# Performance work log

Hardware: AMD Instinct MI355X
Metric: run time of the kernel (lower is better)

Reference implementation:

```python
import jax, jax.numpy as jnp
import numpy as np

B, S, D = 4, 512, 256
H_SP, W_SP = 64, 64
NUM_HEADS = 8
HEAD_DIM = D // NUM_HEADS


def setup_inputs() -> dict:
    key = jax.random.key(0)
    ks = jax.random.split(key, 10)
    scale = 1.0 / np.sqrt(D)
    return {
        "query": jax.random.normal(ks[0], (B, S, D), dtype=jnp.float32),
        "key_value": jax.random.normal(ks[1], (B, D, H_SP, W_SP), dtype=jnp.float32),
        "Wq": jax.random.normal(ks[2], (D, D), dtype=jnp.float32) * scale,
        "bq": jnp.zeros((D,), dtype=jnp.float32),
        "Wk": jax.random.normal(ks[3], (D, D), dtype=jnp.float32) * scale,
        "bk": jnp.zeros((D,), dtype=jnp.float32),
        "Wv": jax.random.normal(ks[4], (D, D), dtype=jnp.float32) * scale,
        "bv": jnp.zeros((D,), dtype=jnp.float32),
        "Wo": jax.random.normal(ks[5], (D, D), dtype=jnp.float32) * scale,
        "bo": jnp.zeros((D,), dtype=jnp.float32),
    }


def reference(query, key_value, Wq, bq, Wk, bk, Wv, bv, Wo, bo):
    # query: (B, S, D); key_value: (B, D, H, W)
    b, d, h, w = key_value.shape
    s = query.shape[1]
    hw = h * w
    kv = key_value.reshape(b, d, hw).transpose(0, 2, 1)  # (B, HW, D)

    # Linear projections (torch Linear: x @ W.T + b)
    Q = query @ Wq.T + bq                                # (B, S, D)
    K = kv @ Wk.T + bk                                   # (B, HW, D)
    V = kv @ Wv.T + bv                                   # (B, HW, D)

    # Split heads: (B, nH, len, hd)
    Qh = Q.reshape(b, s, NUM_HEADS, HEAD_DIM).transpose(0, 2, 1, 3)
    Kh = K.reshape(b, hw, NUM_HEADS, HEAD_DIM).transpose(0, 2, 1, 3)
    Vh = V.reshape(b, hw, NUM_HEADS, HEAD_DIM).transpose(0, 2, 1, 3)

    scale = HEAD_DIM ** -0.5
    # NOTE: _add_spatial_attention is dead code (returns attn unchanged);
    # norm1/norm2 are never applied in forward; dropout is identity in eval.
    attn = jnp.einsum('bhsd,bhkd->bhsk', Qh, Kh) * scale  # (B, nH, S, HW)
    attn = jax.nn.softmax(attn, axis=-1)
    out = jnp.einsum('bhsk,bhkd->bhsd', attn, Vh)         # (B, nH, S, hd)
    out = out.transpose(0, 2, 1, 3).reshape(b, s, d)      # (B, S, D)
    return out @ Wo.T + bo
```

## Files before the change

kernel.cpp:

```cpp
#include <hip/hip_runtime.h>

constexpr int B_  = 4;
constexpr int S_  = 512;
constexpr int D_  = 256;
constexpr int HW_ = 4096;
constexpr int NH_ = 8;
constexpr int HD_ = 32;
constexpr int NSPLIT = 4;
constexpr int ROWS_  = B_ * NH_ * S_;
constexpr int KVB    = 64;
constexpr int TILES  = HW_ / NSPLIT / KVB;

typedef float  f32x4   __attribute__((ext_vector_type(4)));
typedef float  f32x16  __attribute__((ext_vector_type(16)));
typedef short  s16x4   __attribute__((ext_vector_type(4)));
typedef short  s16x8   __attribute__((ext_vector_type(8)));
typedef __bf16 bf16x8  __attribute__((ext_vector_type(8)));
typedef unsigned int u32x2 __attribute__((ext_vector_type(2)));
typedef unsigned int u32x4 __attribute__((ext_vector_type(4)));

__device__ __forceinline__ f32x4 mfma_bf16(s16x8 a, s16x8 b, f32x4 c) {
  return __builtin_amdgcn_mfma_f32_16x16x32_bf16(
      __builtin_bit_cast(bf16x8, a), __builtin_bit_cast(bf16x8, b), c, 0, 0, 0);
}
__device__ __forceinline__ f32x16 mfma32(s16x8 a, s16x8 b, f32x16 c) {
  return __builtin_amdgcn_mfma_f32_32x32x16_bf16(
      __builtin_bit_cast(bf16x8, a), __builtin_bit_cast(bf16x8, b), c, 0, 0, 0);
}

__device__ __forceinline__ void split4(float4 v, s16x4& h, s16x4& l) {
  float x[4] = {v.x, v.y, v.z, v.w};
  #pragma unroll
  for (int j = 0; j < 4; ++j) {
    unsigned xb = __float_as_uint(x[j]);
    h[j] = (short)(xb >> 16);
    float lo = x[j] - __uint_as_float(xb & 0xFFFF0000u);
    l[j] = (short)((__float_as_uint(lo) + 0x8000u) >> 16);
  }
}

__device__ __forceinline__ unsigned pk_hi(float x, float y) {
  return (__float_as_uint(x) >> 16) | (__float_as_uint(y) & 0xFFFF0000u);
}
__device__ __forceinline__ unsigned pk_lo(float x, float y) {
  float rx = x - __uint_as_float(__float_as_uint(x) & 0xFFFF0000u);
  float ry = y - __uint_as_float(__float_as_uint(y) & 0xFFFF0000u);
  return (__float_as_uint(rx) >> 16) | (__float_as_uint(ry) & 0xFFFF0000u);
}

__global__ __launch_bounds__(256)
void transpose_split(const float* __restrict__ KV,
                     short* __restrict__ Th, short* __restrict__ Tl)
{
  __shared__ float tile[64][65];
  const int bid = blockIdx.x;
  const int hwb = bid & 63;
  const int db  = (bid >> 6) & 3;
  const int b   = bid >> 8;
  const int hw0 = hwb * 64, d0 = db * 64;
  const int tid = threadIdx.x;
  #pragma unroll
  for (int i = 0; i < 4; ++i) {
    const int idx = tid + (i << 8);
    const int d = idx >> 4, h4 = idx & 15;
    *(float4*)&tile[d][h4 * 4] =
        *(const float4*)&KV[((size_t)(b * D_ + d0 + d)) * HW_ + hw0 + h4 * 4];
  }
  __syncthreads();
  #pragma unroll
  for (int i = 0; i < 4; ++i) {
    const int idx = tid + (i << 8);
    const int hw = idx >> 4, d4 = idx & 15;
    const float4 v = make_float4(tile[d4*4+0][hw], tile[d4*4+1][hw],
                                 tile[d4*4+2][hw], tile[d4*4+3][hw]);
    s16x4 hh, ll; split4(v, hh, ll);
    const size_t o = ((size_t)(b * HW_ + hw0 + hw)) * D_ + d0 + d4 * 4;
    *(s16x4*)&Th[o] = hh; *(s16x4*)&Tl[o] = ll;
  }
}

template<bool ASPLIT, bool DUAL, bool OSPLIT>
__global__ __launch_bounds__(256)
void gemm_mfma(const float* __restrict__ Af,
               const short* __restrict__ Ah_, const short* __restrict__ Al_,
               const float* __restrict__ W0, const float* __restrict__ b0,
               float* __restrict__ C0f, short* __restrict__ C0h, short* __restrict__ C0l,
               const float* __restrict__ W1, const float* __restrict__ b1,
               short* __restrict__ C1h, short* __restrict__ C1l,
               int M, float alpha)
{
  union Sm {
    struct {
      short Ah[64][40], Al[64][40];
      short W0h[64][40], W0l[64][40];
      short W1h[64][40], W1l[64][40];
    } s;
    float ep[64][76];
  };
  __shared__ __align__(16) Sm sm;

  const int tid = threadIdx.x;
  const int wv = tid >> 6, lane = tid & 63, lq = lane & 15, lg = lane >> 4;
  const int wm = wv >> 1, wn = wv & 1;
  const int nx = M >> 6;
  int bid = blockIdx.x;
  bid = (bid & 7) * ((nx << 2) >> 3) + (bid >> 3);
  const int xm = bid % nx, yn = bid / nx;
  const int m0 = xm << 6, n0 = yn << 6;

  f32x4 acc0[2][2] = {};
  f32x4 acc1[2][2] = {};

  s16x8 aH, aL;
  float4 aF[2], w0R[2], w1R[2];

  auto gload = [&](int kt) {
    const int k0 = kt << 5;
    if constexpr (ASPLIT) {
      const int m = tid >> 2, c8 = tid & 3;
      const size_t off = (size_t)(m0 + m) * D_ + k0 + c8 * 8;
      aH = *(const s16x8*)&Ah_[off];
      aL = *(const s16x8*)&Al_[off];
    } else {
      #pragma unroll
      for (int i = 0; i < 2; ++i) {
        const int idx = tid + (i << 8);
        const int m = idx >> 3, c4 = idx & 7;
        aF[i] = *(const float4*)&Af[(size_t)(m0 + m) * D_ + k0 + c4 * 4];
      }
    }
    #pragma unroll
    for (int i = 0; i < 2; ++i) {
      const int idx = tid + (i << 8);
      const int n = idx >> 3, c4 = idx & 7;
      w0R[i] = *(const float4*)&W0[(size_t)(n0 + n) * D_ + k0 + c4 * 4];
      if constexpr (DUAL)
        w1R[i] = *(const float4*)&W1[(size_t)(n0 + n) * D_ + k0 + c4 * 4];
    }
  };

  auto stage = [&]() {
    if constexpr (ASPLIT) {
      const int m = tid >> 2, c8 = tid & 3;
      *(s16x8*)&sm.s.Ah[m][c8 * 8] = aH;
      *(s16x8*)&sm.s.Al[m][c8 * 8] = aL;
    } else {
      #pragma unroll
      for (int i = 0; i < 2; ++i) {
        const int idx = tid + (i << 8);
        const int m = idx >> 3, c4 = idx & 7;
        s16x4 hh, ll; split4(aF[i], hh, ll);
        *(s16x4*)&sm.s.Ah[m][c4 * 4] = hh;
        *(s16x4*)&sm.s.Al[m][c4 * 4] = ll;
      }
    }
    #pragma unroll
    for (int i = 0; i < 2; ++i) {
      const int idx = tid + (i << 8);
      const int n = idx >> 3, c4 = idx & 7;
      float4 w = w0R[i];
      w.x *= alpha; w.y *= alpha; w.z *= alpha; w.w *= alpha;
      s16x4 hh, ll; split4(w, hh, ll);
      *(s16x4*)&sm.s.W0h[n][c4 * 4] = hh;
      *(s16x4*)&sm.s.W0l[n][c4 * 4] = ll;
      if constexpr (DUAL) {
        split4(w1R[i], hh, ll);
        *(s16x4*)&sm.s.W1h[n][c4 * 4] = hh;
        *(s16x4*)&sm.s.W1l[n][c4 * 4] = ll;
      }
    }
  };

  gload(0);
  #pragma unroll
  for (int kt = 0; kt < 8; ++kt) {
    __syncthreads();
    stage();
    __syncthreads();
    if (kt < 7) gload(kt + 1);
    s16x8 ah[2], al[2];
    #pragma unroll
    for (int mi = 0; mi < 2; ++mi) {
      ah[mi] = *(const s16x8*)&sm.s.Ah[wm * 32 + mi * 16 + lq][lg * 8];
      al[mi] = *(const s16x8*)&sm.s.Al[wm * 32 + mi * 16 + lq][lg * 8];
    }
    #pragma unroll
    for (int ni = 0; ni < 2; ++ni) {
      const int nr = wn * 32 + ni * 16 + lq;
      const s16x8 bh = *(const s16x8*)&sm.s.W0h[nr][lg * 8];
      const s16x8 bl = *(const s16x8*)&sm.s.W0l[nr][lg * 8];
      #pragma unroll
      for (int mi = 0; mi < 2; ++mi) {
        acc0[mi][ni] = mfma_bf16(ah[mi], bh, acc0[mi][ni]);
        acc0[mi][ni] = mfma_bf16(al[mi], bh, acc0[mi][ni]);
        acc0[mi][ni] = mfma_bf16(ah[mi], bl, acc0[mi][ni]);
      }
      if constexpr (DUAL) {
        const s16x8 ch = *(const s16x8*)&sm.s.W1h[nr][lg * 8];
        const s16x8 cl = *(const s16x8*)&sm.s.W1l[nr][lg * 8];
        #pragma unroll
        for (int mi = 0; mi < 2; ++mi) {
          acc1[mi][ni] = mfma_bf16(ah[mi], ch, acc1[mi][ni]);
          acc1[mi][ni] = mfma_bf16(al[mi], ch, acc1[mi][ni]);
          acc1[mi][ni] = mfma_bf16(ah[mi], cl, acc1[mi][ni]);
        }
      }
    }
  }

  __syncthreads();
  #pragma unroll
  for (int mi = 0; mi < 2; ++mi)
    #pragma unroll
    for (int ni = 0; ni < 2; ++ni)
      #pragma unroll
      for (int r = 0; r < 4; ++r)
        sm.ep[wm*32 + mi*16 + lg*4 + r][wn*32 + ni*16 + lq] = acc0[mi][ni][r];
  __syncthreads();
  #pragma unroll
  for (int i = 0; i < 4; ++i) {
    const int idx = tid + (i << 8);
    const int m = idx >> 4, c4 = idx & 15;
    const float4 v = *(const float4*)&sm.ep[m][c4 * 4];
    const float4 bb = *(const float4*)&b0[n0 + c4 * 4];
    const float4 o = make_float4(v.x + alpha * bb.x, v.y + alpha * bb.y,
                                 v.z + alpha * bb.z, v.w + alpha * bb.w);
    const size_t off = (size_t)(m0 + m) * D_ + n0 + c4 * 4;
    if constexpr (OSPLIT) {
      s16x4 hh, ll; split4(o, hh, ll);
      *(s16x4*)&C0h[off] = hh;
      *(s16x4*)&C0l[off] = ll;
    } else {
      *(float4*)&C0f[off] = o;
    }
  }

  if constexpr (DUAL) {
    __syncthreads();
    #pragma unroll
    for (int mi = 0; mi < 2; ++mi)
      #pragma unroll
      for (int ni = 0; ni < 2; ++ni)
        *(f32x4*)&sm.ep[wn*32 + ni*16 + lq][wm*32 + mi*16 + lg*4] = acc1[mi][ni];
    __syncthreads();
    const int b = m0 >> 12, hw0 = m0 & (HW_ - 1);
    #pragma unroll
    for (int i = 0; i < 4; ++i) {
      const int idx = tid + (i << 8);
      const int n = idx >> 4, m4 = idx & 15;
      const float4 v = *(const float4*)&sm.ep[n][m4 * 4];
      const float bb = b1[n0 + n];
      const float4 o = make_float4(v.x + bb, v.y + bb, v.z + bb, v.w + bb);
      s16x4 hh, ll; split4(o, hh, ll);
      const size_t off = ((size_t)(b * D_ + n0 + n)) * HW_ + hw0 + m4 * 4;
      *(s16x4*)&C1h[off] = hh;
      *(s16x4*)&C1l[off] = ll;
    }
  }
}

__global__ __launch_bounds__(256)
void attn_mfma32(const short* __restrict__ Qh_, const short* __restrict__ Ql_,
                 const short* __restrict__ Kh_, const short* __restrict__ Kl_,
                 const short* __restrict__ Vth, const short* __restrict__ Vtl,
                 float* __restrict__ Opart, float* __restrict__ Ml)
{
  union Sm {
    short V[2][2][32][72];
    float ep[4][32][33];
  };
  __shared__ __align__(16) Sm sm;

  const int tid  = threadIdx.x;
  const int wv   = tid >> 6, lane = tid & 63;
  const int lq   = lane & 31, hi = lane >> 5;

  int w = blockIdx.x;
  w = (w & 7) * 64 + (w >> 3);
  const int qt = w & 3;
  const int h  = (w >> 2) & 7;
  const int b  = (w >> 5) & 3;
  const int sp = w >> 7;
  const int q0 = qt * 128 + wv * 32;

  s16x8 qh[2], ql[2];
  {
    const size_t qb = ((size_t)(b * S_ + q0 + lq)) * D_ + h * HD_ + hi * 8;
    qh[0] = *(const s16x8*)&Qh_[qb];      qh[1] = *(const s16x8*)&Qh_[qb + 16];
    ql[0] = *(const s16x8*)&Ql_[qb];      ql[1] = *(const s16x8*)&Ql_[qb + 16];
  }

  f32x16 o = {0.f,0.f,0.f,0.f, 0.f,0.f,0.f,0.f, 0.f,0.f,0.f,0.f, 0.f,0.f,0.f,0.f};
  float mrun = -1e30f, lrun = 0.f;

  const int dd = tid >> 3, c8 = tid & 7;
  s16x8 vrH, vrL;
  auto gloadV = [&](int t) {
    const size_t a = ((size_t)(b * D_ + h * HD_ + dd)) * HW_ + (size_t)t * KVB + c8 * 8;
    vrH = *(const s16x8*)&Vth[a];
    vrL = *(const s16x8*)&Vtl[a];
  };
  auto writeV = [&](int p) {
    *(s16x8*)&sm.V[p][0][dd][c8 * 8] = vrH;
    *(s16x8*)&sm.V[p][1][dd][c8 * 8] = vrL;
  };

  int p = 0;
  gloadV(sp * TILES);
  writeV(0);

  for (int tt = 0; tt < TILES; ++tt) {
    const int t = sp * TILES + tt;
    if (tt + 1 < TILES) gloadV(t + 1);
    __syncthreads();

    f32x16 sc[2];
    #pragma unroll
    for (int cc = 0; cc < 2; ++cc) {
      const size_t kb = ((size_t)(b * HW_ + t * KVB + cc * 32 + lq)) * D_ + h * HD_ + hi * 8;
      const s16x8 kh0 = *(const s16x8*)&Kh_[kb];
      const s16x8 kh1 = *(const s16x8*)&Kh_[kb + 16];
      const s16x8 kl0 = *(const s16x8*)&Kl_[kb];
      const s16x8 kl1 = *(const s16x8*)&Kl_[kb + 16];
      f32x16 a = {0.f,0.f,0.f,0.f, 0.f,0.f,0.f,0.f, 0.f,0.f,0.f,0.f, 0.f,0.f,0.f,0.f};
      a = mfma32(kh0, qh[0], a);
      a = mfma32(kh1, qh[1], a);
      a = mfma32(kl0, qh[0], a);
      a = mfma32(kl1, qh[1], a);
      a = mfma32(kh0, ql[0], a);
      a = mfma32(kh1, ql[1], a);
      sc[cc] = a;
    }

    float mt = sc[0][0];
    #pragma unroll
    for (int cc = 0; cc < 2; ++cc)
      #pragma unroll
      for (int r = 0; r < 16; ++r) mt = fmaxf(mt, sc[cc][r]);
    mt = fmaxf(mt, __shfl_xor(mt, 32));
    const float nm = fmaxf(mrun, mt);
    const float fr = __expf(mrun - nm);
    mrun = nm;
    o *= fr;
    float ps = 0.f;
    #pragma unroll
    for (int cc = 0; cc < 2; ++cc)
      #pragma unroll
      for (int r = 0; r < 16; ++r) {
        const float e = __expf(sc[cc][r] - nm);
        sc[cc][r] = e;
        ps += e;
      }
    ps += __shfl_xor(ps, 32);
    lrun = lrun * fr + ps;

    #pragma unroll
    for (int wn = 0; wn < 4; ++wn) {
      const int cc = wn >> 1, base = (wn & 1) * 8;
      const unsigned a_h = pk_hi(sc[cc][base+0], sc[cc][base+1]);
      const unsigned b_h = pk_hi(sc[cc][base+4], sc[cc][base+5]);
      const unsigned c_h = pk_hi(sc[cc][base+2], sc[cc][base+3]);
      const unsigned d_h = pk_hi(sc[cc][base+6], sc[cc][base+7]);
      const unsigned a_l = pk_lo(sc[cc][base+0], sc[cc][base+1]);
      const unsigned b_l = pk_lo(sc[cc][base+4], sc[cc][base+5]);
      const unsigned c_l = pk_lo(sc[cc][base+2], sc[cc][base+3]);
      const unsigned d_l = pk_lo(sc[cc][base+6], sc[cc][base+7]);
      const u32x2 s1 = __builtin_amdgcn_permlane32_swap(a_h, b_h, false, false);
      const u32x2 s2 = __builtin_amdgcn_permlane32_swap(c_h, d_h, false, false);
      const u32x2 s3 = __builtin_amdgcn_permlane32_swap(a_l, b_l, false, false);
      const u32x2 s4 = __builtin_amdgcn_permlane32_swap(c_l, d_l, false, false);
      const u32x4 wH = {s1[0], s2[0], s1[1], s2[1]};
      const u32x4 wL = {s3[0], s4[0], s3[1], s4[1]};
      const s16x8 pH = __builtin_bit_cast(s16x8, wH);
      const s16x8 pL = __builtin_bit_cast(s16x8, wL);
      const s16x8 vh = *(const s16x8*)&sm.V[p][0][lq][wn * 16 + hi * 8];
      const s16x8 vl = *(const s16x8*)&sm.V[p][1][lq][wn * 16 + hi * 8];
      o = mfma32(vh, pH, o);
      o = mfma32(vl, pH, o);
      o = mfma32(vh, pL, o);
    }

    if (tt + 1 < TILES) writeV(p ^ 1);
    p ^= 1;
  }

  __syncthreads();
  if (lane < 32) {
    const int g = (b * NH_ + h) * S_ + q0 + lq;
    Ml[((size_t)sp * ROWS_ + g) * 2 + 0] = mrun;
    Ml[((size_t)sp * ROWS_ + g) * 2 + 1] = lrun;
  }
  #pragma unroll
  for (int r = 0; r < 16; ++r) {
    const int d = (r & 3) + 8 * (r >> 2) + 4 * hi;
    sm.ep[wv][lq][d] = o[r];
  }
  const int qq = lane >> 1, d0 = (lane & 1) * 16;
  const int g2 = (b * NH_ + h) * S_ + q0 + qq;
  float* dst = &Opart[((size_t)sp * ROWS_ + g2) * HD_ + d0];
  #pragma unroll
  for (int j = 0; j < 4; ++j)
    *(float4*)(dst + j * 4) = *(const float4*)&sm.ep[wv][qq][d0 + j * 4];
}

__global__ __launch_bounds__(256)
void attn_combine(const float* __restrict__ Opart, const float* __restrict__ Ml,
                  short* __restrict__ AOh, short* __restrict__ AOl)
{
  const int idx = blockIdx.x * 256 + threadIdx.x;
  const int g  = idx >> 3;
  const int c4 = idx & 7;

  float M = -1e30f;
  #pragma unroll
  for (int s = 0; s < NSPLIT; ++s)
    M = fmaxf(M, Ml[((size_t)s * ROWS_ + g) * 2]);

  float4 acc = make_float4(0.f, 0.f, 0.f, 0.f);
  float L = 0.f;
  #pragma unroll
  for (int s = 0; s < NSPLIT; ++s) {
    const size_t base = (size_t)s * ROWS_ + g;
    const float w = __expf(Ml[base * 2] - M);
    L += Ml[base * 2 + 1] * w;
    const float4 o = *(const float4*)&Opart[base * HD_ + c4 * 4];
    acc.x += o.x * w; acc.y += o.y * w; acc.z += o.z * w; acc.w += o.w * w;
  }
  const float inv = 1.0f / L;

  const int q  = g & (S_ - 1);
  const int bh = g >> 9;
  const int h  = bh & (NH_ - 1);
  const int b  = bh >> 3;
  const float4 r = make_float4(acc.x * inv, acc.y * inv, acc.z * inv, acc.w * inv);
  s16x4 hh, ll; split4(r, hh, ll);
  const size_t o = (size_t)(b * S_ + q) * D_ + h * HD_ + c4 * 4;
  *(s16x4*)&AOh[o] = hh;
  *(s16x4*)&AOl[o] = ll;
}

extern "C" void kernel_launch(void* const* d_in, const int* in_sizes, int n_in,
                              void* d_out, int out_size, void* d_ws, size_t ws_size,
                              hipStream_t stream)
{
  const float* query = (const float*)d_in[0];
  const float* keyva = (const float*)d_in[1];
  const float* Wq = (const float*)d_in[2];
  const float* bq = (const float*)d_in[3];
  const float* Wk = (const float*)d_in[4];
  const float* bk = (const float*)d_in[5];
  const float* Wv = (const float*)d_in[6];
  const float* bv = (const float*)d_in[7];
  const float* Wo = (const float*)d_in[8];
  const float* bo = (const float*)d_in[9];
  float* out = (float*)d_out;

  char* w = (char*)d_ws;
  short* KvtH = (short*)w; w += 8388608;
  short* KvtL = (short*)w; w += 8388608;
  short* Qh   = (short*)w; w += 1048576;
  short* Ql   = (short*)w; w += 1048576;
  short* Kh   = (short*)w; w += 8388608;
  short* Kl   = (short*)w; w += 8388608;
  short* VtH  = (short*)w; w += 8388608;
  short* VtL  = (short*)w; w += 8388608;
  short* AOh  = (short*)w; w += 1048576;
  short* AOl  = (short*)w; w += 1048576;
  float* Opart= (float*)KvtH;
  float* Ml   = (float*)KvtL;

  const dim3 blk(256);
  const float qscale = 0.17677669529663687f;

  transpose_split<<<dim3(1024), blk, 0, stream>>>(keyva, KvtH, KvtL);

  gemm_mfma<true, true, true><<<dim3(1024), blk, 0, stream>>>(
      nullptr, KvtH, KvtL, Wk, bk, nullptr, Kh, Kl, Wv, bv, VtH, VtL,
      B_ * HW_, 1.0f);

  gemm_mfma<false, false, true><<<dim3(128), blk, 0, stream>>>(
      query, nullptr, nullptr, Wq, bq, nullptr, Qh, Ql, nullptr, nullptr,
      nullptr, nullptr, B_ * S_, qscale);

  attn_mfma32<<<dim3(NSPLIT * B_ * NH_ * (S_ / 128)), blk, 0, stream>>>(
      Qh, Ql, Kh, Kl, VtH, VtL, Opart, Ml);

  attn_combine<<<dim3(ROWS_ * HD_ / 4 / 256), blk, 0, stream>>>(Opart, Ml, AOh, AOl);

  gemm_mfma<true, false, false><<<dim3(128), blk, 0, stream>>>(
      nullptr, AOh, AOl, Wo, bo, out, nullptr, nullptr, nullptr, nullptr,
      nullptr, nullptr, B_ * S_, 1.0f);
}
```

Before: 177.2 us.

## Pre-split K/V weights, double attention splits, use exp2 softmax and MFMA priority

Adds a kernel that splits Wk/Wv into bf16 hi/lo once, so the K/V projection GEMM loads pre-split weights instead of converting floats in every block. Attention KV splits go from 4 to 8 with a 4-waves occupancy bound and a remapped block swizzle. Softmax uses exp2 with log2e folded into the Q scale, tree reductions for the max and sum, and s_setprio around the MFMA groups. Workspace is rearranged so Ml gets its own buffer and AO aliases the VtH buffer. In exchange the combine step reads twice as many partial results and there is one more launch.

Result: no change. 176.8 us (-0.2%).

```diff
diff --git a/kernel.cpp b/kernel.cpp
--- a/kernel.cpp
+++ b/kernel.cpp
@@ -6,7 +6,7 @@
 constexpr int HW_ = 4096;
 constexpr int NH_ = 8;
 constexpr int HD_ = 32;
-constexpr int NSPLIT = 4;
+constexpr int NSPLIT = 8;
 constexpr int ROWS_  = B_ * NH_ * S_;
 constexpr int KVB    = 64;
 constexpr int TILES  = HW_ / NSPLIT / KVB;
@@ -46,6 +46,20 @@
   float rx = x - __uint_as_float(__float_as_uint(x) & 0xFFFF0000u);
   float ry = y - __uint_as_float(__float_as_uint(y) & 0xFFFF0000u);
   return (__float_as_uint(rx) >> 16) | (__float_as_uint(ry) & 0xFFFF0000u);
+}
+
+__global__ __launch_bounds__(256)
+void split_w(const float* __restrict__ Wk, const float* __restrict__ Wv,
+             short* __restrict__ WkH, short* __restrict__ WkL,
+             short* __restrict__ WvH, short* __restrict__ WvL)
+{
+  const int idx = blockIdx.x * 256 + threadIdx.x;
+  const int m = idx >> 14;
+  const int o4 = idx & 16383;
+  const float4 v = *(const float4*)&(m ? Wv : Wk)[o4 * 4];
+  s16x4 hh, ll; split4(v, hh, ll);
+  *(s16x4*)&(m ? WvH : WkH)[o4 * 4] = hh;
+  *(s16x4*)&(m ? WvL : WkL)[o4 * 4] = ll;
 }
 
 __global__ __launch_bounds__(256)
@@ -79,13 +93,16 @@
   }
 }
 
-template<bool ASPLIT, bool DUAL, bool OSPLIT>
+template<bool ASPLIT, bool WSPLIT, bool DUAL, bool OSPLIT>
 __global__ __launch_bounds__(256)
 void gemm_mfma(const float* __restrict__ Af,
                const short* __restrict__ Ah_, const short* __restrict__ Al_,
-               const float* __restrict__ W0, const float* __restrict__ b0,
+               const float* __restrict__ W0f,
+               const short* __restrict__ W0h_, const short* __restrict__ W0l_,
+               const float* __restrict__ b0,
                float* __restrict__ C0f, short* __restrict__ C0h, short* __restrict__ C0l,
-               const float* __restrict__ W1, const float* __restrict__ b1,
+               const short* __restrict__ W1h_, const short* __restrict__ W1l_,
+               const float* __restrict__ b1,
                short* __restrict__ C1h, short* __restrict__ C1l,
                int M, float alpha)
 {
@@ -111,8 +128,8 @@
   f32x4 acc0[2][2] = {};
   f32x4 acc1[2][2] = {};
 
-  s16x8 aH, aL;
-  float4 aF[2], w0R[2], w1R[2];
+  s16x8 aH, aL, w0H, w0L, w1H, w1L;
+  float4 aF[2], w0R[2];
 
   auto gload = [&](int kt) {
     const int k0 = kt << 5;
@@ -129,13 +146,22 @@
         aF[i] = *(const float4*)&Af[(size_t)(m0 + m) * D_ + k0 + c4 * 4];
       }
     }
-    #pragma unroll
-    for (int i = 0; i < 2; ++i) {
-      const int idx = tid + (i << 8);
-      const int n = idx >> 3, c4 = idx & 7;
-      w0R[i] = *(const float4*)&W0[(size_t)(n0 + n) * D_ + k0 + c4 * 4];
-      if constexpr (DUAL)
-        w1R[i] = *(const float4*)&W1[(size_t)(n0 + n) * D_ + k0 + c4 * 4];
+    if constexpr (WSPLIT) {
+      const int n = tid >> 2, c8 = tid & 3;
+      const size_t off = (size_t)(n0 + n) * D_ + k0 + c8 * 8;
+      w0H = *(const s16x8*)&W0h_[off];
+      w0L = *(const s16x8*)&W0l_[off];
+      if constexpr (DUAL) {
+        w1H = *(const s16x8*)&W1h_[off];
+        w1L = *(const s16x8*)&W1l_[off];
+      }
+    } else {
+      #pragma unroll
+      for (int i = 0; i < 2; ++i) {
+        const int idx = tid + (i << 8);
+        const int n = idx >> 3, c4 = idx & 7;
+        w0R[i] = *(const float4*)&W0f[(size_t)(n0 + n) * D_ + k0 + c4 * 4];
+      }
     }
   };
 
@@ -154,19 +180,24 @@
         *(s16x4*)&sm.s.Al[m][c4 * 4] = ll;
       }
     }
-    #pragma unroll
-    for (int i = 0; i < 2; ++i) {
-      const int idx = tid + (i << 8);
-      const int n = idx >> 3, c4 = idx & 7;
-      float4 w = w0R[i];
-      w.x *= alpha; w.y *= alpha; w.z *= alpha; w.w *= alpha;
-      s16x4 hh, ll; split4(w, hh, ll);
-      *(s16x4*)&sm.s.W0h[n][c4 * 4] = hh;
-      *(s16x4*)&sm.s.W0l[n][c4 * 4] = ll;
+    if constexpr (WSPLIT) {
+      const int n = tid >> 2, c8 = tid & 3;
+      *(s16x8*)&sm.s.W0h[n][c8 * 8] = w0H;
+      *(s16x8*)&sm.s.W0l[n][c8 * 8] = w0L;
       if constexpr (DUAL) {
-        split4(w1R[i], hh, ll);
-        *(s16x4*)&sm.s.W1h[n][c4 * 4] = hh;
-        *(s16x4*)&sm.s.W1l[n][c4 * 4] = ll;
+        *(s16x8*)&sm.s.W1h[n][c8 * 8] = w1H;
+        *(s16x8*)&sm.s.W1l[n][c8 * 8] = w1L;
+      }
+    } else {
+      #pragma unroll
+      for (int i = 0; i < 2; ++i) {
+        const int idx = tid + (i << 8);
+        const int n = idx >> 3, c4 = idx & 7;
+        float4 w = w0R[i];
+        w.x *= alpha; w.y *= alpha; w.z *= alpha; w.w *= alpha;
+        s16x4 hh, ll; split4(w, hh, ll);
+        *(s16x4*)&sm.s.W0h[n][c4 * 4] = hh;
+        *(s16x4*)&sm.s.W0l[n][c4 * 4] = ll;
       }
     }
   };
@@ -259,7 +290,7 @@
   }
 }
 
-__global__ __launch_bounds__(256)
+__global__ __launch_bounds__(256, 4)
 void attn_mfma32(const short* __restrict__ Qh_, const short* __restrict__ Ql_,
                  const short* __restrict__ Kh_, const short* __restrict__ Kl_,
                  const short* __restrict__ Vth, const short* __restrict__ Vtl,
@@ -276,7 +307,7 @@
   const int lq   = lane & 31, hi = lane >> 5;
 
   int w = blockIdx.x;
-  w = (w & 7) * 64 + (w >> 3);
+  w = (w & 7) * 128 + (w >> 3);
   const int qt = w & 3;
   const int h  = (w >> 2) & 7;
   const int b  = (w >> 5) & 3;
@@ -323,35 +354,40 @@
       const s16x8 kl0 = *(const s16x8*)&Kl_[kb];
       const s16x8 kl1 = *(const s16x8*)&Kl_[kb + 16];
       f32x16 a = {0.f,0.f,0.f,0.f, 0.f,0.f,0.f,0.f, 0.f,0.f,0.f,0.f, 0.f,0.f,0.f,0.f};
+      __builtin_amdgcn_s_setprio(1);
       a = mfma32(kh0, qh[0], a);
       a = mfma32(kh1, qh[1], a);
       a = mfma32(kl0, qh[0], a);
       a = mfma32(kl1, qh[1], a);
       a = mfma32(kh0, ql[0], a);
       a = mfma32(kh1, ql[1], a);
+      __builtin_amdgcn_s_setprio(0);
       sc[cc] = a;
     }
 
-    float mt = sc[0][0];
-    #pragma unroll
-    for (int cc = 0; cc < 2; ++cc)
-      #pragma unroll
-      for (int r = 0; r < 16; ++r) mt = fmaxf(mt, sc[cc][r]);
-    mt = fmaxf(mt, __shfl_xor(mt, 32));
+    float tr[16];
+    #pragma unroll
+    for (int r = 0; r < 16; ++r) tr[r] = fmaxf(sc[0][r], sc[1][r]);
+    #pragma unroll
+    for (int s = 8; s > 0; s >>= 1)
+      #pragma unroll
+      for (int r = 0; r < s; ++r) tr[r] = fmaxf(tr[r], tr[r + s]);
+    const float mt = fmaxf(tr[0], __shfl_xor(tr[0], 32));
     const float nm = fmaxf(mrun, mt);
-    const float fr = __expf(mrun - nm);
+    const float fr = exp2f(mrun - nm);
     mrun = nm;
     o *= fr;
-    float ps = 0.f;
     #pragma unroll
     for (int cc = 0; cc < 2; ++cc)
       #pragma unroll
-      for (int r = 0; r < 16; ++r) {
-        const float e = __expf(sc[cc][r] - nm);
-        sc[cc][r] = e;
-        ps += e;
-      }
-    ps += __shfl_xor(ps, 32);
+      for (int r = 0; r < 16; ++r) sc[cc][r] = exp2f(sc[cc][r] - nm);
+    #pragma unroll
+    for (int r = 0; r < 16; ++r) tr[r] = sc[0][r] + sc[1][r];
+    #pragma unroll
+    for (int s = 8; s > 0; s >>= 1)
+      #pragma unroll
+      for (int r = 0; r < s; ++r) tr[r] += tr[r + s];
+    const float ps = tr[0] + __shfl_xor(tr[0], 32);
     lrun = lrun * fr + ps;
 
     #pragma unroll
@@ -375,9 +411,11 @@
       const s16x8 pL = __builtin_bit_cast(s16x8, wL);
       const s16x8 vh = *(const s16x8*)&sm.V[p][0][lq][wn * 16 + hi * 8];
       const s16x8 vl = *(const s16x8*)&sm.V[p][1][lq][wn * 16 + hi * 8];
+      __builtin_amdgcn_s_setprio(1);
       o = mfma32(vh, pH, o);
       o = mfma32(vl, pH, o);
       o = mfma32(vh, pL, o);
+      __builtin_amdgcn_s_setprio(0);
     }
 
     if (tt + 1 < TILES) writeV(p ^ 1);
@@ -421,7 +459,7 @@
   #pragma unroll
   for (int s = 0; s < NSPLIT; ++s) {
     const size_t base = (size_t)s * ROWS_ + g;
-    const float w = __expf(Ml[base * 2] - M);
+    const float w = exp2f(Ml[base * 2] - M);
     L += Ml[base * 2 + 1] * w;
     const float4 o = *(const float4*)&Opart[base * HD_ + c4 * 4];
     acc.x += o.x * w; acc.y += o.y * w; acc.z += o.z * w; acc.w += o.w * w;
@@ -464,30 +502,35 @@
   short* Kl   = (short*)w; w += 8388608;
   short* VtH  = (short*)w; w += 8388608;
   short* VtL  = (short*)w; w += 8388608;
-  short* AOh  = (short*)w; w += 1048576;
-  short* AOl  = (short*)w; w += 1048576;
+  short* WkH  = (short*)w; w += 262144;
+  short* WkL  = (short*)w; w += 262144;
+  short* WvH  = (short*)w; w += 262144;
+  short* WvL  = (short*)w; w += 262144;
+  float* Ml   = (float*)w; w += 1048576;
   float* Opart= (float*)KvtH;
-  float* Ml   = (float*)KvtL;
+  short* AOh  = VtH;
+  short* AOl  = VtH + 524288;
 
   const dim3 blk(256);
-  const float qscale = 0.17677669529663687f;
-
+  const float qscale = 0.17677669529663687f * 1.4426950408889634f;
+
+  split_w<<<dim3(128), blk, 0, stream>>>(Wk, Wv, WkH, WkL, WvH, WvL);
   transpose_split<<<dim3(1024), blk, 0, stream>>>(keyva, KvtH, KvtL);
 
-  gemm_mfma<true, true, true><<<dim3(1024), blk, 0, stream>>>(
-      nullptr, KvtH, KvtL, Wk, bk, nullptr, Kh, Kl, Wv, bv, VtH, VtL,
-      B_ * HW_, 1.0f);
-
-  gemm_mfma<false, false, true><<<dim3(128), blk, 0, stream>>>(
-      query, nullptr, nullptr, Wq, bq, nullptr, Qh, Ql, nullptr, nullptr,
-      nullptr, nullptr, B_ * S_, qscale);
+  gemm_mfma<true, true, true, true><<<dim3(1024), blk, 0, stream>>>(
+      nullptr, KvtH, KvtL, nullptr, WkH, WkL, bk, nullptr, Kh, Kl,
+      WvH, WvL, bv, VtH, VtL, B_ * HW_, 1.0f);
+
+  gemm_mfma<false, false, false, true><<<dim3(128), blk, 0, stream>>>(
+      query, nullptr, nullptr, Wq, nullptr, nullptr, bq, nullptr, Qh, Ql,
+      nullptr, nullptr, nullptr, nullptr, nullptr, B_ * S_, qscale);
 
   attn_mfma32<<<dim3(NSPLIT * B_ * NH_ * (S_ / 128)), blk, 0, stream>>>(
       Qh, Ql, Kh, Kl, VtH, VtL, Opart, Ml);
 
   attn_combine<<<dim3(ROWS_ * HD_ / 4 / 256), blk, 0, stream>>>(Opart, Ml, AOh, AOl);
 
-  gemm_mfma<true, false, false><<<dim3(128), blk, 0, stream>>>(
-      nullptr, AOh, AOl, Wo, bo, out, nullptr, nullptr, nullptr, nullptr,
-      nullptr, nullptr, B_ * S_, 1.0f);
-}
+  gemm_mfma<true, false, false, false><<<dim3(128), blk, 0, stream>>>(
+      nullptr, AOh, AOl, Wo, nullptr, nullptr, bo, out, nullptr, nullptr,
+      nullptr, nullptr, nullptr, nullptr, nullptr, B_ * S_, 1.0f);
+}
```
